# Kernel tuning notes

Hardware: AMD Instinct MI355X
Metric: run time of the kernel (lower is better)

The kernel has to match this reference:

```python
import jax, jax.numpy as jnp
import numpy as np

HEADS = 4
HEAD_DIM = 32
DIM = 256
HIDDEN = HEADS * HEAD_DIM  # 128
SCALE = HEAD_DIM ** -0.5


def rmsnorm(x, g):
    # channel-wise L2 normalize (dim=1) * g * sqrt(C), lucidrains-style RMSNorm for conv maps
    inv = jax.lax.rsqrt(jnp.sum(x * x, axis=1, keepdims=True) + 1e-12)
    return x * inv * (g * (x.shape[1] ** 0.5))[None, :, None, None]


def setup_inputs() -> dict:
    key = jax.random.key(0)
    k1, k2, k3 = jax.random.split(key, 3)
    b, H, W = 16, 64, 64
    x = jax.random.normal(k1, (b, DIM, H, W), dtype=jnp.float32)
    W_qkv = jax.random.normal(k2, (3 * HIDDEN, DIM), dtype=jnp.float32) * (DIM ** -0.5)
    W_out = jax.random.normal(k3, (DIM, HIDDEN), dtype=jnp.float32) * (HIDDEN ** -0.5)
    b_out = jnp.zeros((DIM,), dtype=jnp.float32)
    g_norm = jnp.ones((DIM,), dtype=jnp.float32)
    g_out = jnp.ones((DIM,), dtype=jnp.float32)
    return {"x": x, "W_qkv": W_qkv, "W_out": W_out, "b_out": b_out,
            "g_norm": g_norm, "g_out": g_out}


def reference(x, W_qkv, W_out, b_out, g_norm, g_out):
    b, c, H, W = x.shape
    n = H * W
    xn = rmsnorm(x, g_norm)
    # 1x1 conv projection to q,k,v: (b, 3*hidden, H, W)
    qkv = jnp.einsum('bchw,oc->bohw', xn, W_qkv)
    qkv = qkv.reshape(b, 3, HEADS, HEAD_DIM, n)
    q, k, v = qkv[:, 0], qkv[:, 1], qkv[:, 2]  # (b, h, d, n)
    q = jax.nn.softmax(q, axis=-2)  # over head_dim
    k = jax.nn.softmax(k, axis=-1)  # over tokens
    # context: (b, h, d, e)
    context = jnp.einsum('bhdn,bhen->bhde', k, v)
    out = jnp.einsum('bhde,bhdn->bhen', context, q) * SCALE  # (b, h, e, n)
    out = out.reshape(b, HIDDEN, H, W)
    out = jnp.einsum('bchw,oc->bohw', out, W_out) + b_out[None, :, None, None]
    return rmsnorm(out, g_out)
```

## Files before the change

### kernel.cpp

```cpp
#include <hip/hip_runtime.h>


typedef _Float16 half8 __attribute__((ext_vector_type(8)));
typedef _Float16 half4 __attribute__((ext_vector_type(4)));
typedef float f32x4 __attribute__((ext_vector_type(4)));

#define SCALE_F 0.17677669529663687f

__global__ __launch_bounds__(256) void kW(const float* __restrict__ W_qkv,
                                          const float* __restrict__ W_out,
                                          const float* __restrict__ g_norm,
                                          _Float16* __restrict__ W16,
                                          _Float16* __restrict__ Wo16) {
  const int t = threadIdx.x;
  __shared__ float g16s[256];
  g16s[t] = g_norm[t] * 16.0f;
  __syncthreads();
  #pragma unroll
  for (int i = 0; i < 8; ++i) {
    int idx = blockIdx.x * 2048 + i * 256 + t;
    if (idx < 24576) {
      f32x4 v = *(const f32x4*)(W_qkv + (size_t)idx * 4);
      int c0 = (idx & 63) * 4;
      half4 h = {(_Float16)(v[0] * g16s[c0]), (_Float16)(v[1] * g16s[c0 + 1]),
                 (_Float16)(v[2] * g16s[c0 + 2]), (_Float16)(v[3] * g16s[c0 + 3])};
      *(half4*)(W16 + (size_t)idx * 4) = h;
    } else {
      f32x4 v = *(const f32x4*)(W_out + (size_t)(idx - 24576) * 4);
      half4 h = {(_Float16)v[0], (_Float16)v[1], (_Float16)v[2], (_Float16)v[3]};
      *(half4*)(Wo16 + (size_t)(idx - 24576) * 4) = h;
    }
  }
}

__global__ __launch_bounds__(256, 3) void k2_mega(const _Float16* __restrict__ W16,
                                                  const float* __restrict__ x,
                                                  _Float16* __restrict__ qhat,
                                                  float* __restrict__ ctxp,
                                                  float* __restrict__ sumep) {
  const int pt = blockIdx.x, b = blockIdx.y;
  const int p0 = pt * 64;
  const int t = threadIdx.x;
  const int h = t >> 6, l = t & 63;
  const int lg = l >> 4, ll = l & 15;
  __shared__ __align__(1024) char smem[50432];
  char* xbuf = smem;
  char* r2 = smem + 32768;
  char* vt = smem;
  float* psum = (float*)(smem + 49152);
  float* sinvp = (float*)(smem + 50176);

  {
    const float* xb = x + ((size_t)b * 256) * 4096 + p0 + l;
    float rsum = 0.f;
    #pragma unroll
    for (int it = 0; it < 16; ++it) {
      int ch0 = it * 16 + h * 4;
      const float* xc = xb + (size_t)ch0 * 4096;
      float v0 = xc[0];
      float v1 = xc[4096];
      float v2 = xc[8192];
      float v3 = xc[12288];
      half4 hv = {(_Float16)v0, (_Float16)v1, (_Float16)v2, (_Float16)v3};
      #pragma unroll
      for (int j = 0; j < 4; ++j) { float f = (float)hv[j]; rsum += f * f; }
      int c = it * 2 + (h >> 1);
      int swz = c ^ (l & 15) ^ (((l >> 4) & 1) << 4);
      *(half4*)(xbuf + l * 512 + (swz << 4) + (h & 1) * 8) = hv;
    }
    psum[l * 4 + h] = rsum;
  }
  half8 af[8][2];
  #pragma unroll
  for (int ks = 0; ks < 8; ++ks)
    #pragma unroll
    for (int mf = 0; mf < 2; ++mf)
      af[ks][mf] = *(const half8*)(W16 + (size_t)(h * 32 + mf * 16 + ll) * 256 + ks * 32 + lg * 8);
  __syncthreads();
  if (t < 64)
    sinvp[t] = rsqrtf(psum[t * 4] + psum[t * 4 + 1] + psum[t * 4 + 2] + psum[t * 4 + 3] + 1e-12f);
  __syncthreads();
  float sv[4];
  #pragma unroll
  for (int nf = 0; nf < 4; ++nf) sv[nf] = sinvp[nf * 16 + ll];

  const f32x4 fz = {0.f, 0.f, 0.f, 0.f};
  #pragma unroll
  for (int mt = 0; mt < 3; ++mt) {
    f32x4 acc[2][4];
    #pragma unroll
    for (int i = 0; i < 2; ++i)
      #pragma unroll
      for (int j = 0; j < 4; ++j) acc[i][j] = fz;
    #pragma unroll
    for (int ks = 0; ks < 8; ++ks) {
      half8 bf[4];
      #pragma unroll
      for (int nf = 0; nf < 4; ++nf)
        bf[nf] = *(const half8*)(xbuf + (nf * 16 + ll) * 512 +
                                 ((((ks * 4 + lg) ^ ll) ^ ((nf & 1) << 4)) << 4));
      #pragma unroll
      for (int mf = 0; mf < 2; ++mf)
        #pragma unroll
        for (int nf = 0; nf < 4; ++nf)
          acc[mf][nf] = __builtin_amdgcn_mfma_f32_16x16x32_f16(af[ks][mf], bf[nf], acc[mf][nf], 0, 0, 0);
    }
    if (mt < 2) {
      const _Float16* Wn = W16 + (size_t)((mt + 1) * 128 + h * 32) * 256;
      #pragma unroll
      for (int ks = 0; ks < 8; ++ks)
        #pragma unroll
        for (int mf = 0; mf < 2; ++mf)
          af[ks][mf] = *(const half8*)(Wn + (size_t)(mf * 16 + ll) * 256 + ks * 32 + lg * 8);
    }
    if (mt == 0) {
      float s[4] = {0.f, 0.f, 0.f, 0.f};
      #pragma unroll
      for (int mf = 0; mf < 2; ++mf)
        #pragma unroll
        for (int nf = 0; nf < 4; ++nf)
          #pragma unroll
          for (int rr = 0; rr < 4; ++rr) {
            float v = __expf(acc[mf][nf][rr] * sv[nf]);
            acc[mf][nf][rr] = v;
            s[nf] += v;
          }
      #pragma unroll
      for (int nf = 0; nf < 4; ++nf) {
        s[nf] += __shfl_xor(s[nf], 16);
        s[nf] += __shfl_xor(s[nf], 32);
        s[nf] = 1.0f / s[nf];
      }
      #pragma unroll
      for (int mf = 0; mf < 2; ++mf)
        #pragma unroll
        for (int nf = 0; nf < 4; ++nf) {
          int px = nf * 16 + ll;
          int cphys = (h * 4 + mf * 2 + (lg >> 1)) ^ (px & 15);
          half4 hv;
          #pragma unroll
          for (int rr = 0; rr < 4; ++rr) hv[rr] = (_Float16)(acc[mf][nf][rr] * s[nf]);
          *(half4*)(r2 + px * 256 + (cphys << 4) + (lg & 1) * 8) = hv;
        }
      __syncthreads();
      _Float16* qb = qhat + ((size_t)b * 4096 + p0) * 128;
      #pragma unroll
      for (int i = 0; i < 4; ++i) {
        int q = i * 256 + t;
        int px = q >> 4, g = q & 15;
        half8 hv = *(const half8*)(r2 + px * 256 + ((g ^ (px & 15)) << 4));
        *(half8*)(qb + (size_t)px * 128 + g * 8) = hv;
      }
      __syncthreads();
    } else if (mt == 1) {
      float rs[2][4];
      #pragma unroll
      for (int mf = 0; mf < 2; ++mf)
        #pragma unroll
        for (int rr = 0; rr < 4; ++rr) rs[mf][rr] = 0.f;
      #pragma unroll
      for (int mf = 0; mf < 2; ++mf)
        #pragma unroll
        for (int nf = 0; nf < 4; ++nf)
          #pragma unroll
          for (int rr = 0; rr < 4; ++rr) {
            float v = __expf(acc[mf][nf][rr] * sv[nf] - 10.f);
            acc[mf][nf][rr] = v;
            rs[mf][rr] += v;
          }
      #pragma unroll
      for (int mf = 0; mf < 2; ++mf)
        #pragma unroll
        for (int rr = 0; rr < 4; ++rr) {
          float v = rs[mf][rr];
          v += __shfl_xor(v, 1);
          v += __shfl_xor(v, 2);
          v += __shfl_xor(v, 4);
          v += __shfl_xor(v, 8);
          rs[mf][rr] = v;
        }
      if (ll == 0) {
        #pragma unroll
        for (int mf = 0; mf < 2; ++mf)
          #pragma unroll
          for (int rr = 0; rr < 4; ++rr)
            sumep[((size_t)b * 128 + h * 32 + mf * 16 + lg * 4 + rr) * 64 + pt] = rs[mf][rr];
      }
      #pragma unroll
      for (int mf = 0; mf < 2; ++mf)
        #pragma unroll
        for (int nf = 0; nf < 4; ++nf)
          #pragma unroll
          for (int rr = 0; rr < 4; ++rr) {
            int ch = h * 32 + mf * 16 + lg * 4 + rr;
            int px = nf * 16 + ll;
            *(_Float16*)(r2 + ch * 128 + (((px >> 3) ^ (ch & 7)) << 4) + (px & 7) * 2) =
                (_Float16)acc[mf][nf][rr];
          }
    } else {
      __syncthreads();
      #pragma unroll
      for (int mf = 0; mf < 2; ++mf)
        #pragma unroll
        for (int nf = 0; nf < 4; ++nf)
          #pragma unroll
          for (int rr = 0; rr < 4; ++rr) {
            int ch = h * 32 + mf * 16 + lg * 4 + rr;
            int px = nf * 16 + ll;
            *(_Float16*)(vt + ch * 128 + (((px >> 3) ^ (ch & 7)) << 4) + (px & 7) * 2) =
                (_Float16)(acc[mf][nf][rr] * sv[nf]);
          }
      f32x4 ca[2][2] = {{fz, fz}, {fz, fz}};
      #pragma unroll
      for (int ks2 = 0; ks2 < 2; ++ks2) {
        half8 a2[2], b2[2];
        #pragma unroll
        for (int ti = 0; ti < 2; ++ti) {
          int ra = h * 32 + ti * 16 + ll;
          int cc = (ks2 * 4 + lg) ^ (ra & 7);
          a2[ti] = *(const half8*)(r2 + ra * 128 + (cc << 4));
          b2[ti] = *(const half8*)(vt + ra * 128 + (cc << 4));
        }
        #pragma unroll
        for (int ti = 0; ti < 2; ++ti)
          #pragma unroll
          for (int tj = 0; tj < 2; ++tj)
            ca[ti][tj] = __builtin_amdgcn_mfma_f32_16x16x32_f16(a2[ti], b2[tj], ca[ti][tj], 0, 0, 0);
      }
      float* cp = ctxp + (size_t)(((b * 64 + pt) * 4) + h) * 1024;
      #pragma unroll
      for (int ti = 0; ti < 2; ++ti)
        #pragma unroll
        for (int tj = 0; tj < 2; ++tj)
          #pragma unroll
          for (int rr = 0; rr < 4; ++rr)
            cp[(ti * 16 + lg * 4 + rr) * 32 + tj * 16 + ll] = ca[ti][tj][rr];
    }
  }
}

__global__ __launch_bounds__(256) void k3_reduce(const float* __restrict__ ctxp,
                                                 const float* __restrict__ sumep,
                                                 float* __restrict__ ctx,
                                                 float* __restrict__ sume) {
  const int sl = blockIdx.x, b = blockIdx.y;
  const int t = threadIdx.x;
  if (sl == 0 && t < 128) {
    float s = 0.f;
    const float* sp = sumep + ((size_t)b * 128 + t) * 64;
    #pragma unroll 8
    for (int pt = 0; pt < 64; ++pt) s += sp[pt];
    sume[b * 128 + t] = s;
  }
  float a = 0.f;
  const float* p = ctxp + (size_t)b * 64 * 4096 + sl * 256 + t;
  #pragma unroll 8
  for (int pt = 0; pt < 64; ++pt) a += p[(size_t)pt * 4096];
  ctx[(size_t)b * 4096 + sl * 256 + t] = a;
}

__global__ __launch_bounds__(256) void k4b_fold(const _Float16* __restrict__ Wo16,
                                                const float* __restrict__ ctx,
                                                const float* __restrict__ sumexp,
                                                _Float16* __restrict__ M) {
  const int mq = blockIdx.x, b = blockIdx.y;
  const int t = threadIdx.x;
  const int h = t >> 6, l = t & 63;
  const int m0 = mq * 64;
  const float* cb = ctx + (size_t)(b * 4 + h) * 1024;
  const float* sb = sumexp + b * 128 + h * 32;
  half8 bf[2];
  #pragma unroll
  for (int n0 = 0; n0 < 2; ++n0) {
    int d = n0 * 16 + (l & 15);
    float s = SCALE_F / sb[d];
    const float* ce = cb + d * 32 + (l >> 4) * 8;
    half8 hb;
    #pragma unroll
    for (int j = 0; j < 8; ++j) hb[j] = (_Float16)(ce[j] * s);
    bf[n0] = hb;
  }
  const f32x4 fz = {0.f, 0.f, 0.f, 0.f};
  _Float16* Mb = M + (size_t)(b * 256) * 128;
  #pragma unroll
  for (int mf = 0; mf < 4; ++mf) {
    int row = m0 + mf * 16 + (l & 15);
    half8 af = *(const half8*)(Wo16 + (size_t)row * 128 + h * 32 + (l >> 4) * 8);
    #pragma unroll
    for (int n0 = 0; n0 < 2; ++n0) {
      f32x4 c = __builtin_amdgcn_mfma_f32_16x16x32_f16(af, bf[n0], fz, 0, 0, 0);
      #pragma unroll
      for (int rr = 0; rr < 4; ++rr) {
        int r = m0 + mf * 16 + (l >> 4) * 4 + rr;
        Mb[(size_t)r * 128 + h * 32 + n0 * 16 + (l & 15)] = (_Float16)c[rr];
      }
    }
  }
}

__global__ __launch_bounds__(256) void k5c_out(const _Float16* __restrict__ M,
                                               const _Float16* __restrict__ qhat,
                                               const float* __restrict__ b_out,
                                               const float* __restrict__ g_out,
                                               float* __restrict__ out) {
  const int pt = blockIdx.x, b = blockIdx.y;
  const int p0 = pt * 64;
  const int t = threadIdx.x;
  const int wid = t >> 6, l = t & 63;
  __shared__ __align__(16) char smem[81920];
  float* rp = (float*)smem;
  float* bo = (float*)(smem + 69632);
  float* g16o = (float*)(smem + 70656);
  float* psum = (float*)(smem + 71680);
  float* sinvp = (float*)(smem + 72704);
  const _Float16* Mb = M + (size_t)b * 256 * 128;
  const _Float16* Qb = qhat + ((size_t)b * 4096 + p0) * 128;
  #pragma unroll
  for (int i = 0; i < 16; ++i) {
    int ci = t + 256 * i;
    int r = ci >> 4, c = ci & 15;
    *(half8*)(smem + r * 256 + ((c ^ (r & 15)) << 4)) = *(const half8*)(Mb + (size_t)r * 128 + c * 8);
  }
  #pragma unroll
  for (int i = 0; i < 4; ++i) {
    int ci = t + 256 * i;
    int r = ci >> 4, c = ci & 15;
    *(half8*)(smem + 65536 + r * 256 + ((c ^ (r & 15)) << 4)) = *(const half8*)(Qb + (size_t)r * 128 + c * 8);
  }
  __syncthreads();
  const f32x4 fz = {0.f, 0.f, 0.f, 0.f};
  f32x4 acc[4][4];
  #pragma unroll
  for (int i = 0; i < 4; ++i)
    #pragma unroll
    for (int j = 0; j < 4; ++j) acc[i][j] = fz;
  #pragma unroll
  for (int kk = 0; kk < 4; ++kk) {
    half8 af[4], bf[4];
    int ck = kk * 4 + (l >> 4);
    #pragma unroll
    for (int mf = 0; mf < 4; ++mf) {
      int r = wid * 64 + mf * 16 + (l & 15);
      af[mf] = *(const half8*)(smem + r * 256 + ((ck ^ (r & 15)) << 4));
    }
    #pragma unroll
    for (int nf = 0; nf < 4; ++nf) {
      int r = nf * 16 + (l & 15);
      bf[nf] = *(const half8*)(smem + 65536 + r * 256 + ((ck ^ (r & 15)) << 4));
    }
    #pragma unroll
    for (int mf = 0; mf < 4; ++mf)
      #pragma unroll
      for (int nf = 0; nf < 4; ++nf)
        acc[mf][nf] = __builtin_amdgcn_mfma_f32_16x16x32_f16(af[mf], bf[nf], acc[mf][nf], 0, 0, 0);
  }
  __syncthreads();
  bo[t] = b_out[t];
  g16o[t] = g_out[t] * 16.0f;
  #pragma unroll
  for (int mf = 0; mf < 4; ++mf)
    #pragma unroll
    for (int nf = 0; nf < 4; ++nf)
      #pragma unroll
      for (int rr = 0; rr < 4; ++rr) {
        int r = wid * 64 + mf * 16 + (l >> 4) * 4 + rr;
        int px = nf * 16 + (l & 15);
        rp[r * 68 + px] = acc[mf][nf][rr];
      }
  __syncthreads();
  {
    int px = t & 63, q = t >> 6;
    float s = 0.f;
    #pragma unroll
    for (int i = 0; i < 64; ++i) {
      int r = q * 64 + i;
      float f = rp[r * 68 + px] + bo[r];
      s += f * f;
    }
    psum[px * 4 + q] = s;
  }
  __syncthreads();
  if (t < 64)
    sinvp[t] = rsqrtf(psum[t * 4] + psum[t * 4 + 1] + psum[t * 4 + 2] + psum[t * 4 + 3] + 1e-12f);
  __syncthreads();
  float* ob = out + (size_t)(b * 256) * 4096 + p0;
  #pragma unroll
  for (int i = 0; i < 16; ++i) {
    int idx4 = t + 256 * i;
    int r = idx4 >> 4, px4 = (idx4 & 15) * 4;
    f32x4 v;
    #pragma unroll
    for (int ii = 0; ii < 4; ++ii)
      v[ii] = (rp[r * 68 + px4 + ii] + bo[r]) * sinvp[px4 + ii] * g16o[r];
    *(f32x4*)(ob + (size_t)r * 4096 + px4) = v;
  }
}

extern "C" void kernel_launch(void* const* d_in, const int* in_sizes, int n_in,
                              void* d_out, int out_size, void* d_ws, size_t ws_size,
                              hipStream_t stream) {
  const float* x      = (const float*)d_in[0];
  const float* W_qkv  = (const float*)d_in[1];
  const float* W_out  = (const float*)d_in[2];
  const float* b_out  = (const float*)d_in[3];
  const float* g_norm = (const float*)d_in[4];
  const float* g_out  = (const float*)d_in[5];
  float* out = (float*)d_out;
  char* ws = (char*)d_ws;
  if (ws_size < 35659776) return;

  _Float16* W16   = (_Float16*)(ws);
  _Float16* Wo16  = (_Float16*)(ws + 196608);
  _Float16* qhat  = (_Float16*)(ws + 262144);
  float*    ctx   = (float*)(ws + 17039360);
  float*    sume  = (float*)(ws + 17301504);
  _Float16* M     = (_Float16*)(ws + 17309696);
  float*    ctxp  = (float*)(ws + 18358272);
  float*    sumep = (float*)(ws + 35135488);

  kW<<<16, 256, 0, stream>>>(W_qkv, W_out, g_norm, W16, Wo16);
  k2_mega<<<dim3(64, 16), 256, 0, stream>>>(W16, x, qhat, ctxp, sumep);
  k3_reduce<<<dim3(16, 16), 256, 0, stream>>>(ctxp, sumep, ctx, sume);
  k4b_fold<<<dim3(4, 16), 256, 0, stream>>>(Wo16, ctx, sume, M);
  k5c_out<<<dim3(64, 16), 256, 0, stream>>>(M, qhat, b_out, g_out, out);
}
```

Before: 76.56 us.

## Split k2_mega pixel tile across two waves per head with 512-thread blocks

The fused QKV projection kernel now uses 512 threads, with two waves per head that each handle half of the 64-pixel tile. The x-load loop is split over 8 waves. The weight fragments are no longer kept in registers for the whole projection; they are loaded from global memory for each k-step. Each wave's partial context product is combined through a shared-memory scratch area before the store. The goal is more waves and lower register pressure per block to hide load latency, at the cost of an extra barrier, repeated weight loads and a larger sumep buffer.

After: 99.29 us. 1.3x slower.

```diff
diff --git a/kernel.cpp b/kernel.cpp
--- a/kernel.cpp
+++ b/kernel.cpp
@@ -33,7 +33,7 @@
   }
 }
 
-__global__ __launch_bounds__(256, 3) void k2_mega(const _Float16* __restrict__ W16,
+__global__ __launch_bounds__(512, 6) void k2_mega(const _Float16* __restrict__ W16,
                                                   const float* __restrict__ x,
                                                   _Float16* __restrict__ qhat,
                                                   float* __restrict__ ctxp,
@@ -41,22 +41,23 @@
   const int pt = blockIdx.x, b = blockIdx.y;
   const int p0 = pt * 64;
   const int t = threadIdx.x;
-  const int h = t >> 6, l = t & 63;
+  const int w = t >> 6, l = t & 63;
+  const int h = w >> 1, ph = w & 1;
   const int lg = l >> 4, ll = l & 15;
-  __shared__ __align__(1024) char smem[50432];
+  __shared__ __align__(1024) char smem[51456];
   char* xbuf = smem;
   char* r2 = smem + 32768;
   char* vt = smem;
+  float* scr = (float*)(smem + 16384);
   float* psum = (float*)(smem + 49152);
-  float* sinvp = (float*)(smem + 50176);
+  float* sinvp = (float*)(smem + 51200);
 
   {
-    const float* xb = x + ((size_t)b * 256) * 4096 + p0 + l;
+    const float* xb = x + ((size_t)(b * 256 + w * 32)) * 4096 + p0 + l;
     float rsum = 0.f;
     #pragma unroll
-    for (int it = 0; it < 16; ++it) {
-      int ch0 = it * 16 + h * 4;
-      const float* xc = xb + (size_t)ch0 * 4096;
+    for (int it = 0; it < 8; ++it) {
+      const float* xc = xb + (size_t)it * 4 * 4096;
       float v0 = xc[0];
       float v1 = xc[4096];
       float v2 = xc[8192];
@@ -64,61 +65,58 @@
       half4 hv = {(_Float16)v0, (_Float16)v1, (_Float16)v2, (_Float16)v3};
       #pragma unroll
       for (int j = 0; j < 4; ++j) { float f = (float)hv[j]; rsum += f * f; }
-      int c = it * 2 + (h >> 1);
+      int c = w * 4 + (it >> 1);
       int swz = c ^ (l & 15) ^ (((l >> 4) & 1) << 4);
-      *(half4*)(xbuf + l * 512 + (swz << 4) + (h & 1) * 8) = hv;
-    }
-    psum[l * 4 + h] = rsum;
-  }
-  half8 af[8][2];
-  #pragma unroll
-  for (int ks = 0; ks < 8; ++ks)
-    #pragma unroll
-    for (int mf = 0; mf < 2; ++mf)
-      af[ks][mf] = *(const half8*)(W16 + (size_t)(h * 32 + mf * 16 + ll) * 256 + ks * 32 + lg * 8);
-  __syncthreads();
-  if (t < 64)
-    sinvp[t] = rsqrtf(psum[t * 4] + psum[t * 4 + 1] + psum[t * 4 + 2] + psum[t * 4 + 3] + 1e-12f);
-  __syncthreads();
-  float sv[4];
-  #pragma unroll
-  for (int nf = 0; nf < 4; ++nf) sv[nf] = sinvp[nf * 16 + ll];
+      *(half4*)(xbuf + l * 512 + (swz << 4) + (it & 1) * 8) = hv;
+    }
+    psum[l * 8 + w] = rsum;
+  }
+  __syncthreads();
+  if (t < 64) {
+    float s = 1e-12f;
+    #pragma unroll
+    for (int j = 0; j < 8; ++j) s += psum[t * 8 + j];
+    sinvp[t] = rsqrtf(s);
+  }
+  __syncthreads();
+  float sv[2];
+  #pragma unroll
+  for (int nf = 0; nf < 2; ++nf) sv[nf] = sinvp[(ph * 2 + nf) * 16 + ll];
 
   const f32x4 fz = {0.f, 0.f, 0.f, 0.f};
+  _Float16* qb = qhat + ((size_t)b * 4096 + p0) * 128;
   #pragma unroll
   for (int mt = 0; mt < 3; ++mt) {
-    f32x4 acc[2][4];
+    f32x4 acc[2][2];
     #pragma unroll
     for (int i = 0; i < 2; ++i)
       #pragma unroll
-      for (int j = 0; j < 4; ++j) acc[i][j] = fz;
+      for (int j = 0; j < 2; ++j) acc[i][j] = fz;
+    const _Float16* Wmt = W16 + (size_t)(mt * 128 + h * 32) * 256;
     #pragma unroll
     for (int ks = 0; ks < 8; ++ks) {
-      half8 bf[4];
-      #pragma unroll
-      for (int nf = 0; nf < 4; ++nf)
-        bf[nf] = *(const half8*)(xbuf + (nf * 16 + ll) * 512 +
-                                 ((((ks * 4 + lg) ^ ll) ^ ((nf & 1) << 4)) << 4));
-      #pragma unroll
-      for (int mf = 0; mf < 2; ++mf)
-        #pragma unroll
-        for (int nf = 0; nf < 4; ++nf)
-          acc[mf][nf] = __builtin_amdgcn_mfma_f32_16x16x32_f16(af[ks][mf], bf[nf], acc[mf][nf], 0, 0, 0);
-    }
-    if (mt < 2) {
-      const _Float16* Wn = W16 + (size_t)((mt + 1) * 128 + h * 32) * 256;
-      #pragma unroll
-      for (int ks = 0; ks < 8; ++ks)
-        #pragma unroll
-        for (int mf = 0; mf < 2; ++mf)
-          af[ks][mf] = *(const half8*)(Wn + (size_t)(mf * 16 + ll) * 256 + ks * 32 + lg * 8);
+      half8 af[2], bf[2];
+      #pragma unroll
+      for (int mf = 0; mf < 2; ++mf)
+        af[mf] = *(const half8*)(Wmt + (size_t)(mf * 16 + ll) * 256 + ks * 32 + lg * 8);
+      #pragma unroll
+      for (int nf = 0; nf < 2; ++nf) {
+        int nfg = ph * 2 + nf;
+        bf[nf] = *(const half8*)(xbuf + (nfg * 16 + ll) * 512 +
+                                 ((((ks * 4 + lg) ^ ll) ^ ((nfg & 1) << 4)) << 4));
+      }
+      #pragma unroll
+      for (int mf = 0; mf < 2; ++mf)
+        #pragma unroll
+        for (int nf = 0; nf < 2; ++nf)
+          acc[mf][nf] = __builtin_amdgcn_mfma_f32_16x16x32_f16(af[mf], bf[nf], acc[mf][nf], 0, 0, 0);
     }
     if (mt == 0) {
-      float s[4] = {0.f, 0.f, 0.f, 0.f};
-      #pragma unroll
-      for (int mf = 0; mf < 2; ++mf)
-        #pragma unroll
-        for (int nf = 0; nf < 4; ++nf)
+      float s[2] = {0.f, 0.f};
+      #pragma unroll
+      for (int mf = 0; mf < 2; ++mf)
+        #pragma unroll
+        for (int nf = 0; nf < 2; ++nf)
           #pragma unroll
           for (int rr = 0; rr < 4; ++rr) {
             float v = __expf(acc[mf][nf][rr] * sv[nf]);
@@ -126,7 +124,7 @@
             s[nf] += v;
           }
       #pragma unroll
-      for (int nf = 0; nf < 4; ++nf) {
+      for (int nf = 0; nf < 2; ++nf) {
         s[nf] += __shfl_xor(s[nf], 16);
         s[nf] += __shfl_xor(s[nf], 32);
         s[nf] = 1.0f / s[nf];
@@ -134,8 +132,8 @@
       #pragma unroll
       for (int mf = 0; mf < 2; ++mf)
         #pragma unroll
-        for (int nf = 0; nf < 4; ++nf) {
-          int px = nf * 16 + ll;
+        for (int nf = 0; nf < 2; ++nf) {
+          int px = (ph * 2 + nf) * 16 + ll;
           int cphys = (h * 4 + mf * 2 + (lg >> 1)) ^ (px & 15);
           half4 hv;
           #pragma unroll
@@ -143,10 +141,9 @@
           *(half4*)(r2 + px * 256 + (cphys << 4) + (lg & 1) * 8) = hv;
         }
       __syncthreads();
-      _Float16* qb = qhat + ((size_t)b * 4096 + p0) * 128;
-      #pragma unroll
-      for (int i = 0; i < 4; ++i) {
-        int q = i * 256 + t;
+      #pragma unroll
+      for (int i = 0; i < 2; ++i) {
+        int q = i * 512 + t;
         int px = q >> 4, g = q & 15;
         half8 hv = *(const half8*)(r2 + px * 256 + ((g ^ (px & 15)) << 4));
         *(half8*)(qb + (size_t)px * 128 + g * 8) = hv;
@@ -161,7 +158,7 @@
       #pragma unroll
       for (int mf = 0; mf < 2; ++mf)
         #pragma unroll
-        for (int nf = 0; nf < 4; ++nf)
+        for (int nf = 0; nf < 2; ++nf)
           #pragma unroll
           for (int rr = 0; rr < 4; ++rr) {
             float v = __expf(acc[mf][nf][rr] * sv[nf] - 10.f);
@@ -184,16 +181,17 @@
         for (int mf = 0; mf < 2; ++mf)
           #pragma unroll
           for (int rr = 0; rr < 4; ++rr)
-            sumep[((size_t)b * 128 + h * 32 + mf * 16 + lg * 4 + rr) * 64 + pt] = rs[mf][rr];
-      }
-      #pragma unroll
-      for (int mf = 0; mf < 2; ++mf)
-        #pragma unroll
-        for (int nf = 0; nf < 4; ++nf)
+            sumep[((size_t)b * 128 + h * 32 + mf * 16 + lg * 4 + rr) * 128 + pt * 2 + ph] =
+                rs[mf][rr];
+      }
+      #pragma unroll
+      for (int mf = 0; mf < 2; ++mf)
+        #pragma unroll
+        for (int nf = 0; nf < 2; ++nf)
           #pragma unroll
           for (int rr = 0; rr < 4; ++rr) {
             int ch = h * 32 + mf * 16 + lg * 4 + rr;
-            int px = nf * 16 + ll;
+            int px = (ph * 2 + nf) * 16 + ll;
             *(_Float16*)(r2 + ch * 128 + (((px >> 3) ^ (ch & 7)) << 4) + (px & 7) * 2) =
                 (_Float16)acc[mf][nf][rr];
           }
@@ -202,24 +200,24 @@
       #pragma unroll
       for (int mf = 0; mf < 2; ++mf)
         #pragma unroll
-        for (int nf = 0; nf < 4; ++nf)
+        for (int nf = 0; nf < 2; ++nf)
           #pragma unroll
           for (int rr = 0; rr < 4; ++rr) {
             int ch = h * 32 + mf * 16 + lg * 4 + rr;
-            int px = nf * 16 + ll;
+            int px = (ph * 2 + nf) * 16 + ll;
             *(_Float16*)(vt + ch * 128 + (((px >> 3) ^ (ch & 7)) << 4) + (px & 7) * 2) =
                 (_Float16)(acc[mf][nf][rr] * sv[nf]);
           }
       f32x4 ca[2][2] = {{fz, fz}, {fz, fz}};
-      #pragma unroll
-      for (int ks2 = 0; ks2 < 2; ++ks2) {
+      {
         half8 a2[2], b2[2];
+        int c = ph * 4 + lg;
         #pragma unroll
         for (int ti = 0; ti < 2; ++ti) {
           int ra = h * 32 + ti * 16 + ll;
-          int cc = (ks2 * 4 + lg) ^ (ra & 7);
-          a2[ti] = *(const half8*)(r2 + ra * 128 + (cc << 4));
-          b2[ti] = *(const half8*)(vt + ra * 128 + (cc << 4));
+          int cc = (c ^ (ra & 7)) << 4;
+          a2[ti] = *(const half8*)(r2 + ra * 128 + cc);
+          b2[ti] = *(const half8*)(vt + ra * 128 + cc);
         }
         #pragma unroll
         for (int ti = 0; ti < 2; ++ti)
@@ -227,14 +225,28 @@
           for (int tj = 0; tj < 2; ++tj)
             ca[ti][tj] = __builtin_amdgcn_mfma_f32_16x16x32_f16(a2[ti], b2[tj], ca[ti][tj], 0, 0, 0);
       }
-      float* cp = ctxp + (size_t)(((b * 64 + pt) * 4) + h) * 1024;
-      #pragma unroll
-      for (int ti = 0; ti < 2; ++ti)
-        #pragma unroll
-        for (int tj = 0; tj < 2; ++tj)
-          #pragma unroll
-          for (int rr = 0; rr < 4; ++rr)
-            cp[(ti * 16 + lg * 4 + rr) * 32 + tj * 16 + ll] = ca[ti][tj][rr];
+      if (ph == 1) {
+        #pragma unroll
+        for (int ti = 0; ti < 2; ++ti)
+          #pragma unroll
+          for (int tj = 0; tj < 2; ++tj)
+            #pragma unroll
+            for (int rr = 0; rr < 4; ++rr)
+              scr[h * 1024 + (ti * 16 + lg * 4 + rr) * 32 + tj * 16 + ll] = ca[ti][tj][rr];
+      }
+      __syncthreads();
+      if (ph == 0) {
+        float* cp = ctxp + (size_t)(((b * 64 + pt) * 4) + h) * 1024;
+        #pragma unroll
+        for (int ti = 0; ti < 2; ++ti)
+          #pragma unroll
+          for (int tj = 0; tj < 2; ++tj)
+            #pragma unroll
+            for (int rr = 0; rr < 4; ++rr) {
+              int o = (ti * 16 + lg * 4 + rr) * 32 + tj * 16 + ll;
+              cp[o] = ca[ti][tj][rr] + scr[h * 1024 + o];
+            }
+      }
     }
   }
 }
@@ -247,9 +259,9 @@
   const int t = threadIdx.x;
   if (sl == 0 && t < 128) {
     float s = 0.f;
-    const float* sp = sumep + ((size_t)b * 128 + t) * 64;
+    const float* sp = sumep + ((size_t)b * 128 + t) * 128;
     #pragma unroll 8
-    for (int pt = 0; pt < 64; ++pt) s += sp[pt];
+    for (int pt = 0; pt < 128; ++pt) s += sp[pt];
     sume[b * 128 + t] = s;
   }
   float a = 0.f;
@@ -407,7 +419,7 @@
   const float* g_out  = (const float*)d_in[5];
   float* out = (float*)d_out;
   char* ws = (char*)d_ws;
-  if (ws_size < 35659776) return;
+  if (ws_size < 36184064) return;
 
   _Float16* W16   = (_Float16*)(ws);
   _Float16* Wo16  = (_Float16*)(ws + 196608);
@@ -419,7 +431,7 @@
   float*    sumep = (float*)(ws + 35135488);
 
   kW<<<16, 256, 0, stream>>>(W_qkv, W_out, g_norm, W16, Wo16);
-  k2_mega<<<dim3(64, 16), 256, 0, stream>>>(W16, x, qhat, ctxp, sumep);
+  k2_mega<<<dim3(64, 16), 512, 0, stream>>>(W16, x, qhat, ctxp, sumep);
   k3_reduce<<<dim3(16, 16), 256, 0, stream>>>(ctxp, sumep, ctx, sume);
   k4b_fold<<<dim3(4, 16), 256, 0, stream>>>(Wo16, ctx, sume, M);
   k5c_out<<<dim3(64, 16), 256, 0, stream>>>(M, qhat, b_out, g_out, out);
```

## Vectorize x loads with lane shuffles and double-buffer W fragments in k2_mega

Applied to the files above, without the earlier changes.

The x tile load now issues 16 float4 global loads per thread, all up front, instead of 64 scalar loads. A 4-lane shuffle transpose regroups the values so each thread still writes four consecutive channels of a pixel into the swizzled LDS buffer. The W fragment registers are split into two buffers (afA/afB), so the next phase's weights load while the current phase's epilogue runs, and the mt loop is unrolled by hand through macros. This trades more registers (16 float4 plus a second 8x2 half8 set) for better load coalescing and latency hiding, which risks register pressure against the occupancy target of 3 set in launch_bounds.

After: 77.86 us. Within noise of the previous version (+1.7%).

```diff
diff --git a/kernel.cpp b/kernel.cpp
--- a/kernel.cpp
+++ b/kernel.cpp
@@ -33,6 +33,40 @@
   }
 }
 
+#define LOAD_AF(dst, mtv)                                                            \
+  {                                                                                  \
+    const _Float16* Wm_ = W16 + (size_t)((mtv) * 128 + h * 32) * 256;                \
+    _Pragma("unroll")                                                                \
+    for (int ks = 0; ks < 8; ++ks)                                                   \
+      _Pragma("unroll")                                                              \
+      for (int mf = 0; mf < 2; ++mf)                                                 \
+        dst[ks][mf] = *(const half8*)(Wm_ + (size_t)(mf * 16 + ll) * 256 +           \
+                                      ks * 32 + lg * 8);                             \
+  }
+
+#define GEMM_PHASE(afc)                                                              \
+  {                                                                                  \
+    _Pragma("unroll")                                                                \
+    for (int i = 0; i < 2; ++i)                                                      \
+      _Pragma("unroll")                                                              \
+      for (int j = 0; j < 4; ++j) acc[i][j] = fz;                                    \
+    _Pragma("unroll")                                                                \
+    for (int ks = 0; ks < 8; ++ks) {                                                 \
+      half8 bf[4];                                                                   \
+      _Pragma("unroll")                                                              \
+      for (int nf = 0; nf < 4; ++nf)                                                 \
+        bf[nf] = *(const half8*)(xbuf + (nf * 16 + ll) * 512 +                       \
+                                 ((((ks * 4 + lg) ^ ll) ^ ((nf & 1) << 4)) << 4));   \
+      _Pragma("unroll")                                                              \
+      for (int mf = 0; mf < 2; ++mf)                                                 \
+        _Pragma("unroll")                                                            \
+        for (int nf = 0; nf < 4; ++nf)                                               \
+          acc[mf][nf] =                                                              \
+              __builtin_amdgcn_mfma_f32_16x16x32_f16(afc[ks][mf], bf[nf],            \
+                                                     acc[mf][nf], 0, 0, 0);          \
+    }                                                                                \
+  }
+
 __global__ __launch_bounds__(256, 3) void k2_mega(const _Float16* __restrict__ W16,
                                                   const float* __restrict__ x,
                                                   _Float16* __restrict__ qhat,
@@ -43,6 +77,7 @@
   const int t = threadIdx.x;
   const int h = t >> 6, l = t & 63;
   const int lg = l >> 4, ll = l & 15;
+  const int u = l & 3;
   __shared__ __align__(1024) char smem[50432];
   char* xbuf = smem;
   char* r2 = smem + 32768;
@@ -50,32 +85,37 @@
   float* psum = (float*)(smem + 49152);
   float* sinvp = (float*)(smem + 50176);
 
-  {
-    const float* xb = x + ((size_t)b * 256) * 4096 + p0 + l;
-    float rsum = 0.f;
-    #pragma unroll
-    for (int it = 0; it < 16; ++it) {
-      int ch0 = it * 16 + h * 4;
-      const float* xc = xb + (size_t)ch0 * 4096;
-      float v0 = xc[0];
-      float v1 = xc[4096];
-      float v2 = xc[8192];
-      float v3 = xc[12288];
-      half4 hv = {(_Float16)v0, (_Float16)v1, (_Float16)v2, (_Float16)v3};
-      #pragma unroll
-      for (int j = 0; j < 4; ++j) { float f = (float)hv[j]; rsum += f * f; }
-      int c = it * 2 + (h >> 1);
-      int swz = c ^ (l & 15) ^ (((l >> 4) & 1) << 4);
-      *(half4*)(xbuf + l * 512 + (swz << 4) + (h & 1) * 8) = hv;
-    }
-    psum[l * 4 + h] = rsum;
-  }
-  half8 af[8][2];
-  #pragma unroll
-  for (int ks = 0; ks < 8; ++ks)
-    #pragma unroll
-    for (int mf = 0; mf < 2; ++mf)
-      af[ks][mf] = *(const half8*)(W16 + (size_t)(h * 32 + mf * 16 + ll) * 256 + ks * 32 + lg * 8);
+  f32x4 vx[16];
+  const float* xb = x + ((size_t)(b * 256 + h * 64)) * 4096 + p0 + (l & ~3);
+  #pragma unroll
+  for (int it = 0; it < 16; ++it)
+    vx[it] = *(const f32x4*)(xb + (size_t)(it * 4 + u) * 4096);
+  half8 afA[8][2], afB[8][2];
+  LOAD_AF(afA, 0);
+  float rsum = 0.f;
+  #pragma unroll
+  for (int it = 0; it < 16; ++it) {
+    f32x4 v = vx[it];
+    float sA = __shfl_xor((u & 1) ? v[0] : v[1], 1);
+    float sB = __shfl_xor((u & 1) ? v[2] : v[3], 1);
+    float a0 = (u & 1) ? sA : v[0];
+    float a1 = (u & 1) ? v[1] : sA;
+    float a2 = (u & 1) ? sB : v[2];
+    float a3 = (u & 1) ? v[3] : sB;
+    float sC = __shfl_xor((u & 2) ? a0 : a2, 2);
+    float sD = __shfl_xor((u & 2) ? a1 : a3, 2);
+    float w0 = (u & 2) ? sC : a0;
+    float w1 = (u & 2) ? sD : a1;
+    float w2 = (u & 2) ? a2 : sC;
+    float w3 = (u & 2) ? a3 : sD;
+    half4 hv = {(_Float16)w0, (_Float16)w1, (_Float16)w2, (_Float16)w3};
+    #pragma unroll
+    for (int j = 0; j < 4; ++j) { float f = (float)hv[j]; rsum += f * f; }
+    int c = h * 8 + (it >> 1);
+    int swz = c ^ (l & 15) ^ (((l >> 4) & 1) << 4);
+    *(half4*)(xbuf + l * 512 + (swz << 4) + (it & 1) * 8) = hv;
+  }
+  psum[l * 4 + h] = rsum;
   __syncthreads();
   if (t < 64)
     sinvp[t] = rsqrtf(psum[t * 4] + psum[t * 4 + 1] + psum[t * 4 + 2] + psum[t * 4 + 3] + 1e-12f);
@@ -85,157 +125,139 @@
   for (int nf = 0; nf < 4; ++nf) sv[nf] = sinvp[nf * 16 + ll];
 
   const f32x4 fz = {0.f, 0.f, 0.f, 0.f};
-  #pragma unroll
-  for (int mt = 0; mt < 3; ++mt) {
-    f32x4 acc[2][4];
-    #pragma unroll
-    for (int i = 0; i < 2; ++i)
-      #pragma unroll
-      for (int j = 0; j < 4; ++j) acc[i][j] = fz;
-    #pragma unroll
-    for (int ks = 0; ks < 8; ++ks) {
-      half8 bf[4];
+  f32x4 acc[2][4];
+
+  GEMM_PHASE(afA);
+  LOAD_AF(afB, 1);
+  {
+    float s[4] = {0.f, 0.f, 0.f, 0.f};
+    #pragma unroll
+    for (int mf = 0; mf < 2; ++mf)
       #pragma unroll
       for (int nf = 0; nf < 4; ++nf)
-        bf[nf] = *(const half8*)(xbuf + (nf * 16 + ll) * 512 +
-                                 ((((ks * 4 + lg) ^ ll) ^ ((nf & 1) << 4)) << 4));
+        #pragma unroll
+        for (int rr = 0; rr < 4; ++rr) {
+          float v = __expf(acc[mf][nf][rr] * sv[nf]);
+          acc[mf][nf][rr] = v;
+          s[nf] += v;
+        }
+    #pragma unroll
+    for (int nf = 0; nf < 4; ++nf) {
+      s[nf] += __shfl_xor(s[nf], 16);
+      s[nf] += __shfl_xor(s[nf], 32);
+      s[nf] = 1.0f / s[nf];
+    }
+    #pragma unroll
+    for (int mf = 0; mf < 2; ++mf)
+      #pragma unroll
+      for (int nf = 0; nf < 4; ++nf) {
+        int px = nf * 16 + ll;
+        int cphys = (h * 4 + mf * 2 + (lg >> 1)) ^ (px & 15);
+        half4 hv;
+        #pragma unroll
+        for (int rr = 0; rr < 4; ++rr) hv[rr] = (_Float16)(acc[mf][nf][rr] * s[nf]);
+        *(half4*)(r2 + px * 256 + (cphys << 4) + (lg & 1) * 8) = hv;
+      }
+    __syncthreads();
+    _Float16* qb = qhat + ((size_t)b * 4096 + p0) * 128;
+    #pragma unroll
+    for (int i = 0; i < 4; ++i) {
+      int q = i * 256 + t;
+      int px = q >> 4, g = q & 15;
+      half8 hv = *(const half8*)(r2 + px * 256 + ((g ^ (px & 15)) << 4));
+      *(half8*)(qb + (size_t)px * 128 + g * 8) = hv;
+    }
+    __syncthreads();
+  }
+
+  GEMM_PHASE(afB);
+  LOAD_AF(afA, 2);
+  {
+    float rs[2][4];
+    #pragma unroll
+    for (int mf = 0; mf < 2; ++mf)
+      #pragma unroll
+      for (int rr = 0; rr < 4; ++rr) rs[mf][rr] = 0.f;
+    #pragma unroll
+    for (int mf = 0; mf < 2; ++mf)
+      #pragma unroll
+      for (int nf = 0; nf < 4; ++nf)
+        #pragma unroll
+        for (int rr = 0; rr < 4; ++rr) {
+          float v = __expf(acc[mf][nf][rr] * sv[nf] - 10.f);
+          acc[mf][nf][rr] = v;
+          rs[mf][rr] += v;
+        }
+    #pragma unroll
+    for (int mf = 0; mf < 2; ++mf)
+      #pragma unroll
+      for (int rr = 0; rr < 4; ++rr) {
+        float v = rs[mf][rr];
+        v += __shfl_xor(v, 1);
+        v += __shfl_xor(v, 2);
+        v += __shfl_xor(v, 4);
+        v += __shfl_xor(v, 8);
+        rs[mf][rr] = v;
+      }
+    if (ll == 0) {
       #pragma unroll
       for (int mf = 0; mf < 2; ++mf)
         #pragma unroll
-        for (int nf = 0; nf < 4; ++nf)
-          acc[mf][nf] = __builtin_amdgcn_mfma_f32_16x16x32_f16(af[ks][mf], bf[nf], acc[mf][nf], 0, 0, 0);
-    }
-    if (mt < 2) {
-      const _Float16* Wn = W16 + (size_t)((mt + 1) * 128 + h * 32) * 256;
-      #pragma unroll
-      for (int ks = 0; ks < 8; ++ks)
-        #pragma unroll
-        for (int mf = 0; mf < 2; ++mf)
-          af[ks][mf] = *(const half8*)(Wn + (size_t)(mf * 16 + ll) * 256 + ks * 32 + lg * 8);
-    }
-    if (mt == 0) {
-      float s[4] = {0.f, 0.f, 0.f, 0.f};
-      #pragma unroll
-      for (int mf = 0; mf < 2; ++mf)
-        #pragma unroll
-        for (int nf = 0; nf < 4; ++nf)
-          #pragma unroll
-          for (int rr = 0; rr < 4; ++rr) {
-            float v = __expf(acc[mf][nf][rr] * sv[nf]);
-            acc[mf][nf][rr] = v;
-            s[nf] += v;
-          }
-      #pragma unroll
-      for (int nf = 0; nf < 4; ++nf) {
-        s[nf] += __shfl_xor(s[nf], 16);
-        s[nf] += __shfl_xor(s[nf], 32);
-        s[nf] = 1.0f / s[nf];
+        for (int rr = 0; rr < 4; ++rr)
+          sumep[((size_t)b * 128 + h * 32 + mf * 16 + lg * 4 + rr) * 64 + pt] = rs[mf][rr];
+    }
+    #pragma unroll
+    for (int mf = 0; mf < 2; ++mf)
+      #pragma unroll
+      for (int nf = 0; nf < 4; ++nf)
+        #pragma unroll
+        for (int rr = 0; rr < 4; ++rr) {
+          int ch = h * 32 + mf * 16 + lg * 4 + rr;
+          int px = nf * 16 + ll;
+          *(_Float16*)(r2 + ch * 128 + (((px >> 3) ^ (ch & 7)) << 4) + (px & 7) * 2) =
+              (_Float16)acc[mf][nf][rr];
+        }
+  }
+
+  GEMM_PHASE(afA);
+  {
+    __syncthreads();
+    #pragma unroll
+    for (int mf = 0; mf < 2; ++mf)
+      #pragma unroll
+      for (int nf = 0; nf < 4; ++nf)
+        #pragma unroll
+        for (int rr = 0; rr < 4; ++rr) {
+          int ch = h * 32 + mf * 16 + lg * 4 + rr;
+          int px = nf * 16 + ll;
+          *(_Float16*)(vt + ch * 128 + (((px >> 3) ^ (ch & 7)) << 4) + (px & 7) * 2) =
+              (_Float16)(acc[mf][nf][rr] * sv[nf]);
+        }
+    f32x4 ca[2][2] = {{fz, fz}, {fz, fz}};
+    #pragma unroll
+    for (int ks2 = 0; ks2 < 2; ++ks2) {
+      half8 a2[2], b2[2];
+      #pragma unroll
+      for (int ti = 0; ti < 2; ++ti) {
+        int ra = h * 32 + ti * 16 + ll;
+        int cc = (ks2 * 4 + lg) ^ (ra & 7);
+        a2[ti] = *(const half8*)(r2 + ra * 128 + (cc << 4));
+        b2[ti] = *(const half8*)(vt + ra * 128 + (cc << 4));
       }
       #pragma unroll
-      for (int mf = 0; mf < 2; ++mf)
-        #pragma unroll
-        for (int nf = 0; nf < 4; ++nf) {
-          int px = nf * 16 + ll;
-          int cphys = (h * 4 + mf * 2 + (lg >> 1)) ^ (px & 15);
-          half4 hv;
-          #pragma unroll
-          for (int rr = 0; rr < 4; ++rr) hv[rr] = (_Float16)(acc[mf][nf][rr] * s[nf]);
-          *(half4*)(r2 + px * 256 + (cphys << 4) + (lg & 1) * 8) = hv;
-        }
-      __syncthreads();
-      _Float16* qb = qhat + ((size_t)b * 4096 + p0) * 128;
-      #pragma unroll
-      for (int i = 0; i < 4; ++i) {
-        int q = i * 256 + t;
-        int px = q >> 4, g = q & 15;
-        half8 hv = *(const half8*)(r2 + px * 256 + ((g ^ (px & 15)) << 4));
-        *(half8*)(qb + (size_t)px * 128 + g * 8) = hv;
-      }
-      __syncthreads();
-    } else if (mt == 1) {
-      float rs[2][4];
-      #pragma unroll
-      for (int mf = 0; mf < 2; ++mf)
-        #pragma unroll
-        for (int rr = 0; rr < 4; ++rr) rs[mf][rr] = 0.f;
-      #pragma unroll
-      for (int mf = 0; mf < 2; ++mf)
-        #pragma unroll
-        for (int nf = 0; nf < 4; ++nf)
-          #pragma unroll
-          for (int rr = 0; rr < 4; ++rr) {
-            float v = __expf(acc[mf][nf][rr] * sv[nf] - 10.f);
-            acc[mf][nf][rr] = v;
-            rs[mf][rr] += v;
-          }
-      #pragma unroll
-      for (int mf = 0; mf < 2; ++mf)
-        #pragma unroll
-        for (int rr = 0; rr < 4; ++rr) {
-          float v = rs[mf][rr];
-          v += __shfl_xor(v, 1);
-          v += __shfl_xor(v, 2);
-          v += __shfl_xor(v, 4);
-          v += __shfl_xor(v, 8);
-          rs[mf][rr] = v;
-        }
-      if (ll == 0) {
-        #pragma unroll
-        for (int mf = 0; mf < 2; ++mf)
-          #pragma unroll
-          for (int rr = 0; rr < 4; ++rr)
-            sumep[((size_t)b * 128 + h * 32 + mf * 16 + lg * 4 + rr) * 64 + pt] = rs[mf][rr];
-      }
-      #pragma unroll
-      for (int mf = 0; mf < 2; ++mf)
-        #pragma unroll
-        for (int nf = 0; nf < 4; ++nf)
-          #pragma unroll
-          for (int rr = 0; rr < 4; ++rr) {
-            int ch = h * 32 + mf * 16 + lg * 4 + rr;
-            int px = nf * 16 + ll;
-            *(_Float16*)(r2 + ch * 128 + (((px >> 3) ^ (ch & 7)) << 4) + (px & 7) * 2) =
-                (_Float16)acc[mf][nf][rr];
-          }
-    } else {
-      __syncthreads();
-      #pragma unroll
-      for (int mf = 0; mf < 2; ++mf)
-        #pragma unroll
-        for (int nf = 0; nf < 4; ++nf)
-          #pragma unroll
-          for (int rr = 0; rr < 4; ++rr) {
-            int ch = h * 32 + mf * 16 + lg * 4 + rr;
-            int px = nf * 16 + ll;
-            *(_Float16*)(vt + ch * 128 + (((px >> 3) ^ (ch & 7)) << 4) + (px & 7) * 2) =
-                (_Float16)(acc[mf][nf][rr] * sv[nf]);
-          }
-      f32x4 ca[2][2] = {{fz, fz}, {fz, fz}};
-      #pragma unroll
-      for (int ks2 = 0; ks2 < 2; ++ks2) {
-        half8 a2[2], b2[2];
-        #pragma unroll
-        for (int ti = 0; ti < 2; ++ti) {
-          int ra = h * 32 + ti * 16 + ll;
-          int cc = (ks2 * 4 + lg) ^ (ra & 7);
-          a2[ti] = *(const half8*)(r2 + ra * 128 + (cc << 4));
-          b2[ti] = *(const half8*)(vt + ra * 128 + (cc << 4));
-        }
-        #pragma unroll
-        for (int ti = 0; ti < 2; ++ti)
-          #pragma unroll
-          for (int tj = 0; tj < 2; ++tj)
-            ca[ti][tj] = __builtin_amdgcn_mfma_f32_16x16x32_f16(a2[ti], b2[tj], ca[ti][tj], 0, 0, 0);
-      }
-      float* cp = ctxp + (size_t)(((b * 64 + pt) * 4) + h) * 1024;
-      #pragma unroll
       for (int ti = 0; ti < 2; ++ti)
         #pragma unroll
         for (int tj = 0; tj < 2; ++tj)
-          #pragma unroll
-          for (int rr = 0; rr < 4; ++rr)
-            cp[(ti * 16 + lg * 4 + rr) * 32 + tj * 16 + ll] = ca[ti][tj][rr];
-    }
+          ca[ti][tj] = __builtin_amdgcn_mfma_f32_16x16x32_f16(a2[ti], b2[tj], ca[ti][tj], 0, 0, 0);
+    }
+    float* cp = ctxp + (size_t)(((b * 64 + pt) * 4) + h) * 1024;
+    #pragma unroll
+    for (int ti = 0; ti < 2; ++ti)
+      #pragma unroll
+      for (int tj = 0; tj < 2; ++tj)
+        #pragma unroll
+        for (int rr = 0; rr < 4; ++rr)
+          cp[(ti * 16 + lg * 4 + rr) * 32 + tj * 16 + ll] = ca[ti][tj][rr];
   }
 }
 
```
